# Kernel optimization log

Hardware: AMD Instinct MI355X
Metric: run time of the kernel (lower is better)

## Reference

```python
import jax, jax.numpy as jnp
import numpy as np

N, D, K, R_DIM = 20000, 256, 16, 64
RADIUS = 50.0     # init radius
ALPHA = 2.0       # hardcoded in forward
THRESH = 0.01     # attention_threshold
EPS_LN = 1e-5     # torch LayerNorm default eps


def layer_norm(v, g, b):
    m = jnp.mean(v, axis=-1, keepdims=True)
    var = jnp.mean((v - m) ** 2, axis=-1, keepdims=True)
    return (v - m) / jnp.sqrt(var + EPS_LN) * g + b


def setup_inputs() -> dict:
    key = jax.random.key(0)
    ks = jax.random.split(key, 8)
    x = jax.random.normal(ks[0], (N, D), dtype=jnp.float32)
    # fixed-degree graph: node i has exactly K neighbors
    row = jnp.repeat(jnp.arange(N, dtype=jnp.int32), K)
    col = jax.random.randint(ks[1], (N * K,), 0, N, dtype=jnp.int32)
    edge_index = jnp.stack([row, col], axis=0)
    spatial_coords = jax.random.uniform(ks[2], (N, 2), dtype=jnp.float32) * 100.0
    gamma = jnp.ones((D,), jnp.float32)
    beta_ln = jnp.zeros((D,), jnp.float32)
    W_self = jax.random.normal(ks[3], (D, D), jnp.float32) * 0.05
    b_self = jnp.zeros((D,), jnp.float32)
    W_nei = jax.random.normal(ks[4], (D, D), jnp.float32) * 0.05
    b_nei = jnp.zeros((D,), jnp.float32)
    W_red = jax.random.normal(ks[5], (R_DIM, D), jnp.float32) * 0.05
    b_red = jnp.zeros((R_DIM,), jnp.float32)
    beta_mix = jnp.asarray(0.5, jnp.float32)
    return {"x": x, "spatial_coords": spatial_coords, "gamma": gamma,
            "beta_ln": beta_ln, "W_self": W_self, "b_self": b_self,
            "W_nei": W_nei, "b_nei": b_nei, "W_red": W_red, "b_red": b_red,
            "beta_mix": beta_mix, "edge_index": edge_index}


def reference(x, spatial_coords, gamma, beta_ln, W_self, b_self, W_nei, b_nei,
              W_red, b_red, beta_mix, edge_index):
    col = edge_index[1].reshape(N, K)              # fixed degree K per node
    neighbors = x[col]                             # [N, K, D] gather
    nb_coords = spatial_coords[col]                # [N, K, 2]
    distances = jnp.linalg.norm(spatial_coords[:, None, :] - nb_coords, axis=-1)  # [N, K]

    t = layer_norm(x, gamma, beta_ln)              # [N, D]
    nb = layer_norm(neighbors, gamma, beta_ln)     # [N, K, D]

    s_scores = t @ W_self.T + b_self               # [N, D]
    n_scores = nb @ W_nei.T + b_nei                # [N, K, D]

    dist_w = jnp.exp(-ALPHA * distances / (RADIUS + 1e-8))  # [N, K]
    weighted_n = n_scores * dist_w[..., None]

    combined = jnp.concatenate([s_scores[:, None, :], weighted_n], axis=1)  # [N, K+1, D]
    cw = jax.nn.softmax(combined, axis=1)
    self_w = cw[:, 0, :]
    nb_w = cw[:, 1:, :]
    self_w = jnp.where(jnp.abs(self_w) >= THRESH, self_w, 0.0)
    nb_w = jnp.where(jnp.abs(nb_w) >= THRESH, nb_w, 0.0)

    context = beta_mix * (self_w * t) + (1.0 - beta_mix) * jnp.sum(nb_w * nb, axis=1)
    reduced = jax.nn.leaky_relu(context @ W_red.T + b_red, 0.01)
    # outer forward applies leaky_relu again (dropout is identity in eval)
    return jax.nn.leaky_relu(reduced, 0.01)
```

## Files before the change

### kernel.cpp

```cpp
#include <hip/hip_runtime.h>
#include <cmath>

#define NN 20000
#define DD 256
#define KK 16
#define LDC3 768

typedef __attribute__((ext_vector_type(8))) short short8;
typedef __attribute__((ext_vector_type(4))) float f32x4;
typedef unsigned int u32;
typedef unsigned short bfu;

__device__ __forceinline__ float b2f(bfu u) {
  union { u32 i; float f; } v; v.i = ((u32)u) << 16; return v.f;
}
__device__ __forceinline__ bfu f2b(float f) {
  u32 u = __float_as_uint(f);
  u = (u + 0x7fff + ((u >> 16) & 1)) >> 16;
  return (bfu)u;
}
__device__ __forceinline__ float wave_sum(float v) {
#pragma unroll
  for (int m = 32; m; m >>= 1) v += __shfl_xor(v, m, 64);
  return v;
}
__device__ __forceinline__ void gl_lds16(const void* g, void* l) {
  __builtin_amdgcn_global_load_lds((const __attribute__((address_space(1))) u32*)g,
                                   (__attribute__((address_space(3))) u32*)l, 16, 0, 0);
}
__device__ __forceinline__ float fexp2(float x) { return __builtin_amdgcn_exp2f(x); }
__device__ __forceinline__ float frcp(float x)  { return __builtin_amdgcn_rcpf(x); }

__global__ __launch_bounds__(256) void prep_kernel(
    const float* __restrict__ x, const float* __restrict__ g,
    const float* __restrict__ b, const float* __restrict__ Wself,
    const float* __restrict__ Wnei, const float* __restrict__ Wred,
    bfu* __restrict__ C3, bfu* __restrict__ Wcat, bfu* __restrict__ Wredb) {
  int bid = blockIdx.x;
  if (bid < 5000) {
    int lane = threadIdx.x & 63;
    int row = (bid << 2) + (threadIdx.x >> 6);
    float4 v = ((const float4*)(x + (size_t)row * DD))[lane];
    float mean = wave_sum(v.x + v.y + v.z + v.w) * (1.0f / 256.0f);
    float4 d = make_float4(v.x - mean, v.y - mean, v.z - mean, v.w - mean);
    float var = wave_sum(d.x * d.x + d.y * d.y + d.z * d.z + d.w * d.w) * (1.0f / 256.0f);
    float rstd = 1.0f / sqrtf(var + 1e-5f);
    float4 g4 = ((const float4*)g)[lane];
    float4 b4 = ((const float4*)b)[lane];
    ushort4 ov;
    ov.x = f2b(d.x * rstd * g4.x + b4.x);
    ov.y = f2b(d.y * rstd * g4.y + b4.y);
    ov.z = f2b(d.z * rstd * g4.z + b4.z);
    ov.w = f2b(d.w * rstd * g4.w + b4.w);
    *(ushort4*)(C3 + (size_t)row * LDC3 + 512 + (lane << 2)) = ov;
  } else {
    int idx = (bid - 5000) * 256 + threadIdx.x;
    if (idx < 65536) Wcat[idx] = f2b(Wself[idx]);
    else if (idx < 131072) Wcat[idx] = f2b(Wnei[idx - 65536]);
    else if (idx < 147456) Wredb[idx - 131072] = f2b(Wred[idx - 131072]);
  }
}

__global__ __launch_bounds__(256) void gemm_kernel(
    const bfu* __restrict__ A, const bfu* __restrict__ Bw,
    const float* __restrict__ bias0, const float* __restrict__ bias1,
    bfu* __restrict__ Cout, int M) {
  __shared__ bfu smA[2][128 * 64];
  __shared__ bfu smB[2][128 * 64];
  int tid = threadIdx.x, lane = tid & 63, wid = tid >> 6;
  int m0 = blockIdx.x * 128;
  int nbase = blockIdx.y * 128;
  const bfu* Bt = Bw + (size_t)nbase * 256;
  int wr = wid >> 1, wc = wid & 1;
  int lr = lane & 15, lk = lane >> 4;

  f32x4 acc[4][4];
#pragma unroll
  for (int i = 0; i < 4; ++i)
#pragma unroll
    for (int j = 0; j < 4; ++j) acc[i][j] = (f32x4){0.f, 0.f, 0.f, 0.f};

#define STAGE(buf, kc)                                                           \
  {                                                                              \
    _Pragma("unroll") for (int i = 0; i < 4; ++i) {                              \
      int p = tid + 256 * i; int row = p >> 3; int c = (p & 7) ^ (row & 7);      \
      gl_lds16(A + (size_t)(m0 + row) * LDC3 + (kc) + c * 8, &smA[buf][p * 8]);  \
    }                                                                            \
    _Pragma("unroll") for (int i = 0; i < 4; ++i) {                              \
      int p = tid + 256 * i; int row = p >> 3; int c = (p & 7) ^ (row & 7);      \
      gl_lds16(Bt + (size_t)row * 256 + (kc) + c * 8, &smB[buf][p * 8]);         \
    }                                                                            \
  }

#define COMPUTE(buf)                                                             \
  {                                                                              \
    _Pragma("unroll") for (int h = 0; h < 2; ++h) {                              \
      short8 af[4], bfr[4];                                                      \
      int cc = h * 4 + lk;                                                       \
      _Pragma("unroll") for (int fm = 0; fm < 4; ++fm) {                         \
        int row = wr * 64 + fm * 16 + lr;                                        \
        af[fm] = *(const short8*)&smA[buf][row * 64 + ((cc ^ (row & 7)) << 3)];  \
      }                                                                          \
      _Pragma("unroll") for (int fn = 0; fn < 4; ++fn) {                         \
        int row = wc * 64 + fn * 16 + lr;                                        \
        bfr[fn] = *(const short8*)&smB[buf][row * 64 + ((cc ^ (row & 7)) << 3)]; \
      }                                                                          \
      _Pragma("unroll") for (int fm = 0; fm < 4; ++fm)                           \
        _Pragma("unroll") for (int fn = 0; fn < 4; ++fn)                         \
          acc[fm][fn] = __builtin_amdgcn_mfma_f32_16x16x32_bf16(                 \
              bfr[fn], af[fm], acc[fm][fn], 0, 0, 0);                            \
    }                                                                            \
  }

  STAGE(0, 0);
  __syncthreads();
  STAGE(1, 64);
  COMPUTE(0);
  __syncthreads();
  STAGE(0, 128);
  COMPUTE(1);
  __syncthreads();
  STAGE(1, 192);
  COMPUTE(0);
  __syncthreads();
  COMPUTE(1);
#undef STAGE
#undef COMPUTE

  const float* bias = (nbase < 256) ? (bias0 + nbase) : (bias1 + (nbase - 256));
#pragma unroll
  for (int fm = 0; fm < 4; ++fm) {
    int m = m0 + wr * 64 + fm * 16 + lr;
    if (m >= M) continue;
#pragma unroll
    for (int fn = 0; fn < 4; ++fn) {
      int lc = wc * 64 + fn * 16 + lk * 4;
      float4 bv = *(const float4*)(bias + lc);
      ushort4 ov;
      ov.x = f2b(acc[fm][fn][0] + bv.x);
      ov.y = f2b(acc[fm][fn][1] + bv.y);
      ov.z = f2b(acc[fm][fn][2] + bv.z);
      ov.w = f2b(acc[fm][fn][3] + bv.w);
      *(ushort4*)(Cout + (size_t)m * LDC3 + nbase + lc) = ov;
    }
  }
}

__global__ __launch_bounds__(256) void gather_kernel(
    const bfu* __restrict__ C3, const float* __restrict__ coords,
    const int* __restrict__ col, const float* __restrict__ bmix,
    const bfu* __restrict__ Wred, const float* __restrict__ bred,
    float* __restrict__ out) {
  __shared__ bfu cstage[16][264];
  const float L2E = 1.4426950408889634f;
  int lane = threadIdx.x & 63;
  int w = threadIdx.x >> 6;
  int i0 = blockIdx.x << 2;
  int i = i0 + w;
  float beta = bmix[0];

  int ck = col[i * KK + (lane & 15)];
  float2 ci = ((const float2*)coords)[i];
  float2 cn = ((const float2*)coords)[ck];
  float dx = ci.x - cn.x, dy = ci.y - cn.y;
  float dwv = fexp2((-2.0f * L2E / (50.0f + 1e-8f)) * sqrtf(dx * dx + dy * dy)) * L2E;

  int d = lane << 2;
  const bfu* rowi = C3 + (size_t)i * LDC3;
  ushort4 sv = *(const ushort4*)(rowi + d);
  float4 e0 = make_float4(fexp2(L2E * b2f(sv.x)), fexp2(L2E * b2f(sv.y)),
                          fexp2(L2E * b2f(sv.z)), fexp2(L2E * b2f(sv.w)));
  float4 Z = e0;
  float4 ef[KK];
  ushort4 tn[KK];
#pragma unroll
  for (int k = 0; k < KK; ++k) {
    int cc = __shfl(ck, k, 64);
    float ww = __shfl(dwv, k, 64);
    const bfu* rowc = C3 + (size_t)cc * LDC3;
    ushort4 uv = *(const ushort4*)(rowc + 256 + d);
    tn[k] = *(const ushort4*)(rowc + 512 + d);
    float4 e = make_float4(fexp2(ww * b2f(uv.x)), fexp2(ww * b2f(uv.y)),
                           fexp2(ww * b2f(uv.z)), fexp2(ww * b2f(uv.w)));
    ef[k] = e;
    Z.x += e.x; Z.y += e.y; Z.z += e.z; Z.w += e.w;
  }
  float4 thr = make_float4(0.01f * Z.x, 0.01f * Z.y, 0.01f * Z.z, 0.01f * Z.w);
  ushort4 tv = *(const ushort4*)(rowi + 512 + d);
  float ob = 1.0f - beta;
  float4 ns = make_float4(0.f, 0.f, 0.f, 0.f);
#pragma unroll
  for (int k = 0; k < KK; ++k) {
    float ex = (ef[k].x >= thr.x) ? ef[k].x : 0.f;
    float ey = (ef[k].y >= thr.y) ? ef[k].y : 0.f;
    float ez = (ef[k].z >= thr.z) ? ef[k].z : 0.f;
    float ew = (ef[k].w >= thr.w) ? ef[k].w : 0.f;
    ns.x += ex * b2f(tn[k].x); ns.y += ey * b2f(tn[k].y);
    ns.z += ez * b2f(tn[k].z); ns.w += ew * b2f(tn[k].w);
  }
  float s0x = (e0.x >= thr.x) ? e0.x : 0.f;
  float s0y = (e0.y >= thr.y) ? e0.y : 0.f;
  float s0z = (e0.z >= thr.z) ? e0.z : 0.f;
  float s0w = (e0.w >= thr.w) ? e0.w : 0.f;
  float4 iz = make_float4(frcp(Z.x), frcp(Z.y), frcp(Z.z), frcp(Z.w));
  ushort4 cb;
  cb.x = f2b((beta * s0x * b2f(tv.x) + ob * ns.x) * iz.x);
  cb.y = f2b((beta * s0y * b2f(tv.y) + ob * ns.y) * iz.y);
  cb.z = f2b((beta * s0z * b2f(tv.z) + ob * ns.z) * iz.z);
  cb.w = f2b((beta * s0w * b2f(tv.w) + ob * ns.w) * iz.w);
  *(ushort4*)&cstage[w][d] = cb;
  __syncthreads();

  int lr16 = lane & 15, lk4 = lane >> 4;
  const bfu* wrow = Wred + (size_t)(w * 16 + lr16) * 256 + (lk4 << 3);
  f32x4 racc = (f32x4){0.f, 0.f, 0.f, 0.f};
#pragma unroll
  for (int ks = 0; ks < 8; ++ks) {
    short8 av = *(const short8*)&cstage[lr16][ks * 32 + (lk4 << 3)];
    short8 bv = *(const short8*)(wrow + ks * 32);
    racc = __builtin_amdgcn_mfma_f32_16x16x32_bf16(av, bv, racc, 0, 0, 0);
  }
  if (lane < 16) {
    float bb = bred[w * 16 + lane];
#pragma unroll
    for (int q = 0; q < 4; ++q) {
      float vv = racc[q] + bb;
      vv = (vv > 0.f) ? vv : 0.01f * vv;
      vv = (vv > 0.f) ? vv : 0.01f * vv;
      out[(size_t)(i0 + q) * 64 + w * 16 + lane] = vv;
    }
  }
}

extern "C" void kernel_launch(void* const* d_in, const int* in_sizes, int n_in,
                              void* d_out, int out_size, void* d_ws, size_t ws_size,
                              hipStream_t stream) {
  (void)in_sizes; (void)n_in; (void)out_size; (void)ws_size;
  const float* x       = (const float*)d_in[0];
  const float* coords  = (const float*)d_in[1];
  const float* gamma   = (const float*)d_in[2];
  const float* beta_ln = (const float*)d_in[3];
  const float* W_self  = (const float*)d_in[4];
  const float* b_self  = (const float*)d_in[5];
  const float* W_nei   = (const float*)d_in[6];
  const float* b_nei   = (const float*)d_in[7];
  const float* W_red   = (const float*)d_in[8];
  const float* b_red   = (const float*)d_in[9];
  const float* bmix    = (const float*)d_in[10];
  const int*   edge    = (const int*)d_in[11];
  const int*   col     = edge + (size_t)NN * KK;

  bfu* C3    = (bfu*)d_ws;
  bfu* Wcat  = (bfu*)((char*)d_ws + 30867456);
  bfu* Wredb = (bfu*)((char*)d_ws + 31129600);

  prep_kernel<<<5576, 256, 0, stream>>>(x, gamma, beta_ln, W_self, W_nei, W_red,
                                        C3, Wcat, Wredb);
  gemm_kernel<<<dim3(157, 4), 256, 0, stream>>>(
      C3 + 512, Wcat, b_self, b_nei, C3, NN);
  gather_kernel<<<5000, 256, 0, stream>>>(C3, coords, col, bmix, Wredb, b_red,
                                          (float*)d_out);
}
```

Measured before the change: 160.9 us.

## Hoist neighbor gathers ahead of exp, use readlane, and remap GEMM blocks per XCD

The gather kernel now issues all 32 neighbor row loads up front, broadcasts the neighbor index and distance weight with readlane instead of shuffles, and recomputes exponentials in the second pass rather than keeping 16 float4 values live. This exposes more memory-level parallelism and lowers register pressure, at the cost of twice as many exp instructions. The GEMM switches to a 1D grid with an XCD-aware block remap, so the four N-tiles of one M-tile run on the same XCD and can share the A rows in L2.

```diff
diff --git a/kernel.cpp b/kernel.cpp
--- a/kernel.cpp
+++ b/kernel.cpp
@@ -30,6 +30,9 @@
 }
 __device__ __forceinline__ float fexp2(float x) { return __builtin_amdgcn_exp2f(x); }
 __device__ __forceinline__ float frcp(float x)  { return __builtin_amdgcn_rcpf(x); }
+__device__ __forceinline__ float rdlanef(float v, int l) {
+  return __int_as_float(__builtin_amdgcn_readlane(__float_as_int(v), l));
+}
 
 __global__ __launch_bounds__(256) void prep_kernel(
     const float* __restrict__ x, const float* __restrict__ g,
@@ -67,9 +70,13 @@
     bfu* __restrict__ Cout, int M) {
   __shared__ bfu smA[2][128 * 64];
   __shared__ bfu smB[2][128 * 64];
+  int orig = blockIdx.x;
+  int xcd = orig & 7;
+  int base = (xcd < 4) ? xcd * 79 : 316 + (xcd - 4) * 78;
+  int wgid = base + (orig >> 3);
+  int m0 = (wgid >> 2) * 128;
+  int nbase = (wgid & 3) * 128;
   int tid = threadIdx.x, lane = tid & 63, wid = tid >> 6;
-  int m0 = blockIdx.x * 128;
-  int nbase = blockIdx.y * 128;
   const bfu* Bt = Bw + (size_t)nbase * 256;
   int wr = wid >> 1, wc = wid & 1;
   int lr = lane & 15, lk = lane >> 4;
@@ -168,35 +175,43 @@
   int d = lane << 2;
   const bfu* rowi = C3 + (size_t)i * LDC3;
   ushort4 sv = *(const ushort4*)(rowi + d);
+  ushort4 tv = *(const ushort4*)(rowi + 512 + d);
+
+  ushort4 uvr[KK], tnr[KK];
+#pragma unroll
+  for (int k = 0; k < KK; ++k) {
+    int cc = __builtin_amdgcn_readlane(ck, k);
+    const bfu* rowc = C3 + (size_t)cc * LDC3;
+    uvr[k] = *(const ushort4*)(rowc + 256 + d);
+    tnr[k] = *(const ushort4*)(rowc + 512 + d);
+  }
+
   float4 e0 = make_float4(fexp2(L2E * b2f(sv.x)), fexp2(L2E * b2f(sv.y)),
                           fexp2(L2E * b2f(sv.z)), fexp2(L2E * b2f(sv.w)));
   float4 Z = e0;
-  float4 ef[KK];
-  ushort4 tn[KK];
 #pragma unroll
   for (int k = 0; k < KK; ++k) {
-    int cc = __shfl(ck, k, 64);
-    float ww = __shfl(dwv, k, 64);
-    const bfu* rowc = C3 + (size_t)cc * LDC3;
-    ushort4 uv = *(const ushort4*)(rowc + 256 + d);
-    tn[k] = *(const ushort4*)(rowc + 512 + d);
-    float4 e = make_float4(fexp2(ww * b2f(uv.x)), fexp2(ww * b2f(uv.y)),
-                           fexp2(ww * b2f(uv.z)), fexp2(ww * b2f(uv.w)));
-    ef[k] = e;
-    Z.x += e.x; Z.y += e.y; Z.z += e.z; Z.w += e.w;
+    float sw = rdlanef(dwv, k);
+    Z.x += fexp2(sw * b2f(uvr[k].x));
+    Z.y += fexp2(sw * b2f(uvr[k].y));
+    Z.z += fexp2(sw * b2f(uvr[k].z));
+    Z.w += fexp2(sw * b2f(uvr[k].w));
   }
   float4 thr = make_float4(0.01f * Z.x, 0.01f * Z.y, 0.01f * Z.z, 0.01f * Z.w);
-  ushort4 tv = *(const ushort4*)(rowi + 512 + d);
+
   float ob = 1.0f - beta;
   float4 ns = make_float4(0.f, 0.f, 0.f, 0.f);
 #pragma unroll
   for (int k = 0; k < KK; ++k) {
-    float ex = (ef[k].x >= thr.x) ? ef[k].x : 0.f;
-    float ey = (ef[k].y >= thr.y) ? ef[k].y : 0.f;
-    float ez = (ef[k].z >= thr.z) ? ef[k].z : 0.f;
-    float ew = (ef[k].w >= thr.w) ? ef[k].w : 0.f;
-    ns.x += ex * b2f(tn[k].x); ns.y += ey * b2f(tn[k].y);
-    ns.z += ez * b2f(tn[k].z); ns.w += ew * b2f(tn[k].w);
+    float sw = rdlanef(dwv, k);
+    float ex = fexp2(sw * b2f(uvr[k].x));
+    float ey = fexp2(sw * b2f(uvr[k].y));
+    float ez = fexp2(sw * b2f(uvr[k].z));
+    float ew = fexp2(sw * b2f(uvr[k].w));
+    ns.x += ((ex >= thr.x) ? ex : 0.f) * b2f(tnr[k].x);
+    ns.y += ((ey >= thr.y) ? ey : 0.f) * b2f(tnr[k].y);
+    ns.z += ((ez >= thr.z) ? ez : 0.f) * b2f(tnr[k].z);
+    ns.w += ((ew >= thr.w) ? ew : 0.f) * b2f(tnr[k].w);
   }
   float s0x = (e0.x >= thr.x) ? e0.x : 0.f;
   float s0y = (e0.y >= thr.y) ? e0.y : 0.f;
@@ -256,7 +271,7 @@
 
   prep_kernel<<<5576, 256, 0, stream>>>(x, gamma, beta_ln, W_self, W_nei, W_red,
                                         C3, Wcat, Wredb);
-  gemm_kernel<<<dim3(157, 4), 256, 0, stream>>>(
+  gemm_kernel<<<dim3(628), 256, 0, stream>>>(
       C3 + 512, Wcat, b_self, b_nei, C3, NN);
   gather_kernel<<<5000, 256, 0, stream>>>(C3, coords, col, bmix, Wredb, b_red,
                                           (float*)d_out);
```

Result: no change. 158.2 us (-1.7%).
